# Kernel optimization log

Hardware: AMD Instinct MI355X
Metric: run time of the kernel (lower is better)

The kernel has to match this reference:

```python
import jax, jax.numpy as jnp
import numpy as np

B, S_ENC, S_DEC = 8, 128, 256
E, H = 256, 512
VE = VD = 32000


def _run_layer(x, h0, Wi, bi, Wh, bh):
    # Unidirectional Elman layer: h_t = tanh(i2h(x_t) + h2h(h_{t-1})).
    # i2h is time-independent, so precompute for all steps. x: [B,S,in]
    xi = jnp.einsum('bsi,hi->bsh', x, Wi) + bi
    def step(h, xt):
        h = jnp.tanh(xt + h @ Wh.T + bh)
        return h, h
    hT, ys = jax.lax.scan(step, h0, jnp.swapaxes(xi, 0, 1))
    return jnp.swapaxes(ys, 0, 1), hT  # [B,S,H], [B,H]


def _forward(enc_input, target, floats):
    (enc_emb, enc_Wi1, enc_bi1, enc_Wh1, enc_bh1, enc_Wi2, enc_bi2, enc_Wh2, enc_bh2,
     dec_emb, attn_We, attn_be, attn_Wh, attn_bh, attn_V, attn_bV,
     dec_Wi1, dec_bi1, dec_Wh1, dec_bh1, dec_Wi2, dec_bi2, dec_Wh2, dec_bh2,
     out_W, out_b) = floats
    b = enc_input.shape[0]
    # ---- encoder: 2-layer unidirectional Elman RNN over embedded tokens ----
    x = enc_emb[enc_input]                              # [B,S_enc,E]
    h0 = jnp.zeros((b, H), x.dtype)
    out1, h1 = _run_layer(x, h0, enc_Wi1, enc_bi1, enc_Wh1, enc_bh1)
    # RNNBlock passes layer1's final hidden as layer2's initial hidden
    enc_out, hidden = _run_layer(out1, h1, enc_Wi2, enc_bi2, enc_Wh2, enc_bh2)

    # ---- decoder with Bahdanau attention, teacher forcing always on ----
    # dec input at t=0 is target[:,0]; thereafter target[:,t-1]
    dec_tokens = jnp.concatenate([target[:, :1], target[:, :-1]], axis=1)
    dec_x = dec_emb[dec_tokens]                         # [B,S_dec,E]
    # W_enc_out(enc_output) is constant across decode steps -> precompute
    pre_enc = jnp.einsum('bsh,gh->bsg', enc_out, attn_We) + attn_be  # [B,S_enc,H]

    def dec_step(hidden, emb_t):
        align = jnp.tanh(pre_enc + (hidden @ attn_Wh.T + attn_bh)[:, None, :])
        dots = jnp.einsum('bsh,h->bs', align, attn_V[0]) + attn_bV[0]  # [B,S_enc]
        attn = jax.nn.softmax(dots, axis=-1)
        ctx = jnp.einsum('bs,bsh->bh', attn, enc_out)   # [B,H]
        x_t = jnp.concatenate([emb_t, ctx], axis=-1)    # [B,E+H]
        # decoder RNNBlock with seq_len=1: both layers start from `hidden`
        # chain per RNNBlock semantics (layer2 initial hidden = layer1 final)
        h1 = jnp.tanh(x_t @ dec_Wi1.T + dec_bi1 + hidden @ dec_Wh1.T + dec_bh1)
        h2 = jnp.tanh(h1 @ dec_Wi2.T + dec_bi2 + h1 @ dec_Wh2.T + dec_bh2)
        pred = h2 @ out_W.T + out_b                     # [B,VD]
        return h2, pred

    _, preds = jax.lax.scan(dec_step, hidden, jnp.swapaxes(dec_x, 0, 1))
    return jnp.swapaxes(preds, 0, 1)                    # [B,S_dec,VD]


def setup_inputs() -> dict:
    key = jax.random.key(0)
    it = iter(jax.random.split(key, 40))
    def nrm(shape, s=0.05):
        return (jax.random.normal(next(it), shape) * s).astype(jnp.float32)
    return dict(
        enc_input=jax.random.randint(next(it), (B, S_ENC), 0, VE),
        target=jax.random.randint(next(it), (B, S_DEC), 0, VD),
        enc_emb=nrm((VE, E)),
        enc_Wi1=nrm((H, E)), enc_bi1=nrm((H,)), enc_Wh1=nrm((H, H)), enc_bh1=nrm((H,)),
        enc_Wi2=nrm((H, H)), enc_bi2=nrm((H,)), enc_Wh2=nrm((H, H)), enc_bh2=nrm((H,)),
        dec_emb=nrm((VD, E)),
        attn_We=nrm((H, H)), attn_be=nrm((H,)), attn_Wh=nrm((H, H)), attn_bh=nrm((H,)),
        attn_V=nrm((1, H)), attn_bV=nrm((1,)),
        dec_Wi1=nrm((H, E + H)), dec_bi1=nrm((H,)), dec_Wh1=nrm((H, H)), dec_bh1=nrm((H,)),
        dec_Wi2=nrm((H, H)), dec_bi2=nrm((H,)), dec_Wh2=nrm((H, H)), dec_bh2=nrm((H,)),
        out_W=nrm((VD, H)), out_b=nrm((VD,)),
    )


def reference(enc_input, target, enc_emb, enc_Wi1, enc_bi1, enc_Wh1, enc_bh1,
              enc_Wi2, enc_bi2, enc_Wh2, enc_bh2, dec_emb,
              attn_We, attn_be, attn_Wh, attn_bh, attn_V, attn_bV,
              dec_Wi1, dec_bi1, dec_Wh1, dec_bh1, dec_Wi2, dec_bi2, dec_Wh2, dec_bh2,
              out_W, out_b):
    floats = (enc_emb, enc_Wi1, enc_bi1, enc_Wh1, enc_bh1, enc_Wi2, enc_bi2, enc_Wh2, enc_bh2,
              dec_emb, attn_We, attn_be, attn_Wh, attn_bh, attn_V, attn_bV,
              dec_Wi1, dec_bi1, dec_Wh1, dec_bh1, dec_Wi2, dec_bi2, dec_Wh2, dec_bh2,
              out_W, out_b)
    return _forward(enc_input, target, floats)
```

## Files before the change

kernel.cpp:

```cpp
#include <hip/hip_runtime.h>

#define TPB 256
#define NWG 32
#define B_  8
#define H_  512
#define E_  256
#define SE_ 128
#define SD_ 256
#define WS  530

typedef unsigned short u16;
typedef unsigned int   u32;
typedef __attribute__((ext_vector_type(4))) float f32x4;
typedef __attribute__((ext_vector_type(8))) short short8;
typedef __attribute__((ext_vector_type(2))) _Float16 half2v;

#define SENTU 0x7FC00001u

__device__ __forceinline__ u16 f2b(float f){
  u32 u = __float_as_uint(f);
  u = (u + 0x7fffu + ((u >> 16) & 1u)) >> 16;
  return (u16)u;
}
__device__ __forceinline__ u16 f2h(float f){
  _Float16 h = (_Float16)f;
  return __builtin_bit_cast(unsigned short, h);
}
__device__ __forceinline__ void b2f2(u32 p, float& a, float& b){
  a = __uint_as_float(p << 16);
  b = __uint_as_float(p & 0xffff0000u);
}
__device__ __forceinline__ float ftanh(float x){
  float e = __expf(2.f * x);
  return 1.f - 2.f / (e + 1.f);
}
__device__ __forceinline__ float red16(float v){
  v += __shfl_xor(v, 1); v += __shfl_xor(v, 2);
  v += __shfl_xor(v, 4); v += __shfl_xor(v, 8);
  return v;
}
__device__ __forceinline__ float sentf(){ return __uint_as_float(SENTU); }
__device__ __forceinline__ bool issent(float x){ return __float_as_uint(x) == SENTU; }
__device__ __forceinline__ float dot2h(half2v w, half2v x, float acc){
#if __has_builtin(__builtin_amdgcn_fdot2)
  return __builtin_amdgcn_fdot2(w, x, acc, false);
#else
  return acc + (float)w.x * (float)x.x + (float)w.y * (float)x.y;
#endif
}

__device__ __forceinline__ float gld(const float* p){
  return __hip_atomic_load(p, __ATOMIC_RELAXED, __HIP_MEMORY_SCOPE_AGENT);
}
__device__ __forceinline__ void gst(float* p, float v){
  __hip_atomic_store(p, v, __ATOMIC_RELAXED, __HIP_MEMORY_SCOPE_AGENT);
}

__device__ __forceinline__ int HPX(int slot,int b,int wg,int r){ return ((slot*8+b)*32+wg)*16+r; }
__device__ __forceinline__ int HPB(int slot,int b){ return (slot*8+b)*512; }
__device__ __forceinline__ int PPX(int slot,int b,int wg,int s){ return ((slot*8+b)*32+wg)*128+s; }
__device__ __forceinline__ int PPB(int slot,int b){ return (slot*8+b)*4096; }

__device__ __forceinline__ void pollgather_h(const float* base, half2v* dsth){
  const int tid = threadIdx.x;
  if (tid < 128){
    const float* p = base + tid*4;
    f32x4 v;
    for (;;){
      asm volatile("global_load_dwordx4 %0, %1, off sc0 sc1\n\ts_waitcnt vmcnt(0)"
                   : "=v"(v) : "v"(p) : "memory");
      bool ok = !issent(v.x) && !issent(v.y) && !issent(v.z) && !issent(v.w);
      if (__all(ok)) break;
      __builtin_amdgcn_s_sleep(1);
    }
    half2v h0, h1;
    h0.x = (_Float16)v.x; h0.y = (_Float16)v.y;
    h1.x = (_Float16)v.z; h1.y = (_Float16)v.w;
    dsth[tid*2]     = h0;
    dsth[tid*2 + 1] = h1;
  }
}

struct Inputs {
  const int   *enc_input, *target;
  const float *enc_emb;
  const float *enc_Wi1, *enc_bi1, *enc_Wh1, *enc_bh1;
  const float *enc_Wi2, *enc_bi2, *enc_Wh2, *enc_bh2;
  const float *dec_emb;
  const float *attn_We, *attn_be, *attn_Wh, *attn_bh, *attn_V, *attn_bV;
  const float *dec_Wi1, *dec_bi1, *dec_Wh1, *dec_bh1;
  const float *dec_Wi2, *dec_bi2, *dec_Wh2, *dec_bh2;
  const float *out_W, *out_b;
};
struct Wksp {
  u32*  bar;
  float *hbuf, *h1buf, *h2buf, *partials;
  float *xi1, *xi2, *out1, *encout, *xe;
  u16   *h2all, *wb;
};

constexpr int OFF_A   = 0;
constexpr int OFF_A2  = 17024;
constexpr int OFF_A3  = 34048;
constexpr int OFF_PM  = 51008;
constexpr int OFF_PES = 59200;
constexpr int OFF_STG = 67904;
constexpr int OFF_WRG = 76096;
constexpr int OFF_XVH = 125248;
constexpr int OFF_XV2H= 126272;
constexpr int OFF_ES  = 127296;
constexpr int OFF_QS  = 127808;
constexpr int OFF_VS  = 127872;
constexpr int OFF_B1  = 127936;
constexpr int OFF_B2  = 128000;
constexpr int OFF_BH  = 128064;
constexpr int OFF_BSC = 128128;
constexpr int OFF_SCR = 128192;
constexpr int LDS_BYTES = 128256;

__device__ __forceinline__ void cbar(u32* slots, int wg, u32 target){
  asm volatile("s_waitcnt vmcnt(0)" ::: "memory");
  __syncthreads();
  const int tid = threadIdx.x;
  if (tid < 64){
    if (tid == 0)
      __hip_atomic_store(&slots[wg], target, __ATOMIC_RELAXED, __HIP_MEMORY_SCOPE_AGENT);
    bool done = false;
    do {
      u32 v = __hip_atomic_load(&slots[tid & 31], __ATOMIC_RELAXED, __HIP_MEMORY_SCOPE_AGENT);
      done = (v >= target);
    } while (__ballot(done) != ~0ull);
  }
  __syncthreads();
  asm volatile("" ::: "memory");
}

__device__ void enc_scan(const Wksp& w,
                         const float* __restrict__ Wh, const float* __restrict__ bh,
                         const float* __restrict__ xi, float* __restrict__ outbuf,
                         int b, int wg, u16* WbE, half2v* xvh, float* bscan)
{
  const int tid = threadIdx.x;
  for (int i = tid; i < 16*512; i += TPB){
    int r = i >> 9, j = i & 511;
    WbE[r*WS + j] = f2h(Wh[((size_t)(wg*16 + r))*H_ + j]);
  }
  if (tid < 16) bscan[tid] = bh[wg*16 + tid];
  __syncthreads();
  for (int t = 0; t < SE_; t++){
    pollgather_h(&w.hbuf[HPB(t&3, b)], xvh);
    __syncthreads();
    int r = tid >> 4, sl = tid & 15;
    float acc = 0.f;
    #pragma unroll
    for (int k = 0; k < 16; k++){
      int jj = sl + 16*k;
      acc = dot2h(*(const half2v*)&WbE[r*WS + 2*jj], xvh[jj], acc);
    }
    acc = red16(acc);
    if (sl == 0){
      int row = wg*16 + r;
      float hv = ftanh(xi[((size_t)b*SE_ + t)*H_ + row] + acc + bscan[r]);
      gst(&w.hbuf[HPX((t+1)&3, b, wg, r)], hv);
      gst(&outbuf[((size_t)b*SE_ + t)*H_ + row], hv);
      gst(&w.hbuf[HPX((t+3)&3, b, wg, r)], sentf());
    }
    asm volatile("s_waitcnt vmcnt(0)" ::: "memory");
    __syncthreads();
  }
}

__global__ __launch_bounds__(TPB, 1) void seq2seq_persist(Inputs in, Wksp w)
{
  __shared__ __attribute__((aligned(16))) unsigned char S[LDS_BYTES];
  u16* Wh1s = (u16*)(S + OFF_A);
  u16* Ws2s = (u16*)(S + OFF_A2);
  u16* Wats = (u16*)(S + OFF_A3);
  u16* WaE  = (u16*)(S + OFF_A);
  u16* WbE  = (u16*)(S + OFF_A2);
  float* stgE = (float*)(S + OFF_A3);
  float* Pm   = (float*)(S + OFF_PM);
  float* pes  = (float*)(S + OFF_PES);
  float* STG  = (float*)(S + OFF_STG);
  float* WRG  = (float*)(S + OFF_WRG);
  half2v* xvh  = (half2v*)(S + OFF_XVH);
  half2v* xv2h = (half2v*)(S + OFF_XV2H);
  float* es   = (float*)(S + OFF_ES);
  float* qs   = (float*)(S + OFF_QS);
  float* Vs   = (float*)(S + OFF_VS);
  float* b1s  = (float*)(S + OFF_B1);
  float* b2s  = (float*)(S + OFF_B2);
  float* bhs  = (float*)(S + OFF_BH);
  float* bscan= (float*)(S + OFF_BSC);
  float* scr  = (float*)(S + OFF_SCR);

  const int bid = blockIdx.x;
  const int c = bid & 7, wg = bid >> 3;
  const int b = c;
  const int tid = threadIdx.x;
  u32* slots = w.bar + c*32;
  u32 bt = 0;

  if (tid < 16){
    gst(&w.hbuf[HPX(0, b, wg, tid)], 0.f);
    #pragma unroll
    for (int s2 = 1; s2 < 4; s2++) gst(&w.hbuf[HPX(s2, b, wg, tid)], sentf());
    #pragma unroll
    for (int s2 = 0; s2 < 4; s2++) gst(&w.h1buf[HPX(s2, b, wg, tid)], sentf());
    #pragma unroll
    for (int s2 = 0; s2 < 3; s2++) gst(&w.h2buf[HPX(s2, b, wg, tid)], sentf());
  }
  if (tid < 128){
    #pragma unroll
    for (int s2 = 0; s2 < 3; s2++) gst(&w.partials[PPX(s2, b, wg, tid)], sentf());
  }

  for (int i = tid; i < 16*256; i += TPB){
    int r = i >> 8, j = i & 255;
    WaE[r*264 + j] = f2b(in.enc_Wi1[((size_t)(wg*16 + r))*E_ + j]);
  }
  if (tid < 16) bscan[tid] = in.enc_bi1[wg*16 + tid];
  __syncthreads();
  for (int k0 = 0; k0 < 8; k0++){
    for (int it = 0; it < 16; it++){
      int tok = in.enc_input[b*SE_ + k0*16 + it];
      stgE[it*256 + tid] = in.enc_emb[(size_t)tok*E_ + tid];
    }
    __syncthreads();
    int r = tid & 15, tt = tid >> 4;
    float acc = 0.f;
    #pragma unroll 16
    for (int j = 0; j < 256; j += 2){
      u32 p = *(const u32*)&WaE[r*264 + j];
      float w0, w1; b2f2(p, w0, w1);
      float2 x = *(const float2*)&stgE[tt*256 + j];
      acc += w0*x.x + w1*x.y;
    }
    w.xi1[((size_t)b*SE_ + k0*16 + tt)*H_ + wg*16 + r] = acc + bscan[r];
    __syncthreads();
  }
  cbar(slots, wg, ++bt);

  enc_scan(w, in.enc_Wh1, in.enc_bh1, w.xi1, w.out1, b, wg, WbE, xvh, bscan);
  cbar(slots, wg, ++bt);

  for (int i = tid; i < 16*512; i += TPB){
    int r = i >> 9, j = i & 511;
    WaE[r*522 + j] = f2b(in.enc_Wi2[((size_t)(wg*16 + r))*H_ + j]);
  }
  if (tid < 16){
    bscan[tid] = in.enc_bi2[wg*16 + tid];
    #pragma unroll
    for (int s2 = 1; s2 < 4; s2++) gst(&w.hbuf[HPX(s2, b, wg, tid)], sentf());
  }
  __syncthreads();
  {
    u16* stg2 = (u16*)stgE;
    for (int k0 = 0; k0 < 8; k0++){
      for (int it = 0; it < 16; it++){
        size_t base = ((size_t)b*SE_ + k0*16 + it)*H_;
        stg2[it*512 + tid]       = f2b(gld(&w.out1[base + tid]));
        stg2[it*512 + tid + 256] = f2b(gld(&w.out1[base + tid + 256]));
      }
      __syncthreads();
      int r = tid & 15, tt = tid >> 4;
      float acc = 0.f;
      #pragma unroll 16
      for (int j = 0; j < 512; j += 2){
        u32 p  = *(const u32*)&WaE[r*522 + j];
        u32 s2 = *(const u32*)&stg2[tt*512 + j];
        float w0, w1, s0, s1; b2f2(p, w0, w1); b2f2(s2, s0, s1);
        acc += w0*s0 + w1*s1;
      }
      w.xi2[((size_t)b*SE_ + k0*16 + tt)*H_ + wg*16 + r] = acc + bscan[r];
      __syncthreads();
    }
  }
  cbar(slots, wg, ++bt);

  enc_scan(w, in.enc_Wh2, in.enc_bh2, w.xi2, w.encout, b, wg, WbE, xvh, bscan);
  cbar(slots, wg, ++bt);

  for (int i = tid; i < 16*768; i += TPB)
    WRG[i] = in.dec_Wi1[(size_t)(wg*16 + i/768)*768 + (i - (i/768)*768)];
  for (int tb = 0; tb < 32; tb++){
    __syncthreads();
    for (int i = tid; i < 8*256; i += TPB){
      int tt = tb*8 + (i >> 8);
      int tok = in.target[b*SD_ + (tt == 0 ? 0 : tt - 1)];
      STG[i] = in.dec_emb[(size_t)tok*E_ + (i & 255)];
    }
    __syncthreads();
    int r = tid >> 4, sl = tid & 15;
    for (int t2 = 0; t2 < 8; t2++){
      float acc = 0.f;
      #pragma unroll
      for (int k = 0; k < 8; k++){
        int j = 2*sl + 32*k;
        float2 wv = *(const float2*)&WRG[r*768 + j];
        float2 xx = *(const float2*)&STG[t2*256 + j];
        acc += wv.x*xx.x + wv.y*xx.y;
      }
      acc = red16(acc);
      if (sl == 0) w.xe[((size_t)b*SD_ + tb*8 + t2)*H_ + wg*16 + r] = acc;
    }
  }
  for (int sb = 0; sb < 32; sb++){
    __syncthreads();
    for (int i = tid; i < 4*512; i += TPB)
      STG[i] = gld(&w.encout[((size_t)b*SE_ + sb*4 + (i >> 9))*H_ + (i & 511)]);
    __syncthreads();
    int r = tid >> 4, sl = tid & 15;
    const float* wer = in.attn_We + (size_t)(wg*16 + r)*H_;
    float a0=0.f, a1=0.f, a2=0.f, a3=0.f;
    float p0=0.f, p1=0.f, p2=0.f, p3=0.f;
    #pragma unroll
    for (int k = 0; k < 16; k++){
      int j = 2*sl + 32*k;
      float2 wv = *(const float2*)&wer[j];
      float2 x0 = *(const float2*)&STG[j];
      float2 x1 = *(const float2*)&STG[512 + j];
      float2 x2 = *(const float2*)&STG[1024 + j];
      float2 x3 = *(const float2*)&STG[1536 + j];
      a0 += wv.x*x0.x + wv.y*x0.y;  a1 += wv.x*x1.x + wv.y*x1.y;
      a2 += wv.x*x2.x + wv.y*x2.y;  a3 += wv.x*x3.x + wv.y*x3.y;
      float2 cv = *(const float2*)&WRG[r*768 + 256 + j];
      p0 += cv.x*x0.x + cv.y*x0.y;  p1 += cv.x*x1.x + cv.y*x1.y;
      p2 += cv.x*x2.x + cv.y*x2.y;  p3 += cv.x*x3.x + cv.y*x3.y;
    }
    a0 = red16(a0); a1 = red16(a1); a2 = red16(a2); a3 = red16(a3);
    p0 = red16(p0); p1 = red16(p1); p2 = red16(p2); p3 = red16(p3);
    if (sl == 0){
      float bed = in.attn_be[wg*16 + r];
      pes[(sb*4 + 0)*17 + r] = a0 + bed;
      pes[(sb*4 + 1)*17 + r] = a1 + bed;
      pes[(sb*4 + 2)*17 + r] = a2 + bed;
      pes[(sb*4 + 3)*17 + r] = a3 + bed;
      Pm[r*128 + sb*4 + 0] = p0;  Pm[r*128 + sb*4 + 1] = p1;
      Pm[r*128 + sb*4 + 2] = p2;  Pm[r*128 + sb*4 + 3] = p3;
    }
  }
  __syncthreads();
  for (int i = tid; i < 16*512; i += TPB){
    int r = i >> 9, j = i & 511;
    size_t o = ((size_t)(wg*16 + r))*H_ + j;
    Wh1s[r*WS + j] = f2h(in.dec_Wh1[o]);
    Ws2s[r*WS + j] = f2h(in.dec_Wi2[o] + in.dec_Wh2[o]);
    Wats[r*WS + j] = f2h(in.attn_Wh[o]);
  }
  if (tid < 16){
    int row = wg*16 + tid;
    b1s[tid] = in.dec_bi1[row] + in.dec_bh1[row];
    b2s[tid] = in.dec_bi2[row] + in.dec_bh2[row];
    bhs[tid] = in.attn_bh[row];
    Vs[tid]  = in.attn_V[row];
    float hv = gld(&w.hbuf[HPX(0, b, wg, tid)]);
    gst(&w.h2buf[HPX(3, b, wg, tid)], hv);
  }
  if (tid == 0) scr[8] = in.attn_bV[0];
  cbar(slots, wg, ++bt);
  const float bVv = scr[8];

  {
    pollgather_h(&w.h2buf[HPB(3, b)], xv2h);
    __syncthreads();
    int r = tid >> 4, sl = tid & 15;
    float acc = 0.f;
    #pragma unroll
    for (int k = 0; k < 16; k++){
      int jj = sl + 16*k;
      acc = dot2h(*(const half2v*)&Wats[r*WS + 2*jj], xv2h[jj], acc);
    }
    acc = red16(acc);
    if (sl == 0) qs[r] = acc + bhs[r];
    __syncthreads();
    if (tid < 128){
      float part = 0.f;
      #pragma unroll
      for (int di = 0; di < 16; di++)
        part += Vs[di] * ftanh(pes[tid*17 + di] + qs[di]);
      gst(&w.partials[PPX(3, b, wg, tid)], part);
    }
  }
  cbar(slots, wg, ++bt);

  const int r = tid >> 4, sl = tid & 15;
  for (int t = 0; t < SD_; t++){
    const int sA = (t+3)&3;
    const int sB = t&3;
    const int sP = (t+1)&3;
    pollgather_h(&w.h2buf[HPB(sA, b)], xv2h);
    __syncthreads();
    {
      float aq = 0.f;
      #pragma unroll
      for (int k = 0; k < 16; k++){
        int jj = sl + 16*k;
        aq = dot2h(*(const half2v*)&Wats[r*WS + 2*jj], xv2h[jj], aq);
      }
      aq = red16(aq);
      if (sl == 0) qs[r] = aq + bhs[r];
    }
    __syncthreads();
    if (tid < 128){
      float part = 0.f;
      #pragma unroll
      for (int di = 0; di < 16; di++)
        part += Vs[di] * ftanh(pes[tid*17 + di] + qs[di]);
      gst(&w.partials[PPX(sA, b, wg, tid)], part);
    }
    float ah = 0.f;
    #pragma unroll
    for (int k = 0; k < 16; k++){
      int jj = sl + 16*k;
      ah = dot2h(*(const half2v*)&Wh1s[r*WS + 2*jj], xv2h[jj], ah);
    }
    if (tid < 128){
      const float* pb = &w.partials[PPB(sA, b)];
      float sum;
      for (;;){
        bool ok = true; sum = bVv;
        #pragma unroll
        for (int k = 0; k < 32; k++){
          float x = gld(pb + k*128 + tid);
          ok = ok && !issent(x);
          sum += x;
        }
        if (__all(ok)) break;
        __builtin_amdgcn_s_sleep(1);
      }
      float e = __expf(sum);
      es[tid] = e;
      float d = e;
      d += __shfl_xor(d, 1);  d += __shfl_xor(d, 2);  d += __shfl_xor(d, 4);
      d += __shfl_xor(d, 8);  d += __shfl_xor(d, 16); d += __shfl_xor(d, 32);
      if ((tid & 63) == 0) scr[tid >> 6] = d;
    }
    __syncthreads();
    {
      float rden = 1.f / (scr[0] + scr[1]);
      float accP = 0.f;
      #pragma unroll
      for (int k = 0; k < 8; k++){
        int s = sl + 16*k;
        accP += Pm[r*128 + s] * es[s];
      }
      float tot = red16(ah + accP*rden);
      if (sl == 0){
        int row = wg*16 + r;
        float h1v = ftanh(tot + w.xe[((size_t)b*SD_ + t)*H_ + row] + b1s[r]);
        gst(&w.h1buf[HPX(sB, b, wg, r)], h1v);
        gst(&w.h2buf[HPX(sP, b, wg, r)], sentf());
      }
      if (tid < 128)
        gst(&w.partials[PPX(sP, b, wg, tid)], sentf());
    }
    pollgather_h(&w.h1buf[HPB(sB, b)], xvh);
    __syncthreads();
    {
      float acc = 0.f;
      #pragma unroll
      for (int k = 0; k < 16; k++){
        int jj = sl + 16*k;
        acc = dot2h(*(const half2v*)&Ws2s[r*WS + 2*jj], xvh[jj], acc);
      }
      acc = red16(acc);
      if (sl == 0){
        float h2v = ftanh(acc + b2s[r]);
        int row = wg*16 + r;
        gst(&w.h2buf[HPX(sB, b, wg, r)], h2v);
        w.h2all[((size_t)(b*SD_ + t))*H_ + row] = f2b(h2v);
        gst(&w.h1buf[HPX((t+2)&3, b, wg, r)], sentf());
      }
    }
    asm volatile("s_waitcnt vmcnt(0)" ::: "memory");
    __syncthreads();
  }
}

__global__ void cvt_bf16(const float* __restrict__ src, u16* __restrict__ dst, int n4){
  int idx = blockIdx.x*blockDim.x + threadIdx.x;
  int stride = gridDim.x*blockDim.x;
  for (int i = idx; i < n4; i += stride){
    float4 v = ((const float4*)src)[i];
    ushort4 o;
    o.x = f2b(v.x); o.y = f2b(v.y); o.z = f2b(v.z); o.w = f2b(v.w);
    ((ushort4*)dst)[i] = o;
  }
}

__global__ __launch_bounds__(256, 1) void out_gemm(const u16* __restrict__ A,
    const u16* __restrict__ Bw, const float* __restrict__ bias, float* __restrict__ out)
{
  __shared__ u16 Al[128*32];
  __shared__ u16 Bl[128*32];
  int tid = threadIdx.x;
  int bidm = blockIdx.x & 15, bidn = blockIdx.x >> 4;
  int m0 = bidm*128, n0 = bidn*128;
  int wv = tid >> 6, l = tid & 63;
  int wm = wv >> 1, wn = wv & 1;
  f32x4 acc[4][4] = {};
  for (int k0 = 0; k0 < 512; k0 += 32){
    __syncthreads();
    #pragma unroll
    for (int rd = 0; rd < 2; rd++){
      int ci = rd*256 + wv*64 + l;
      int row = ci >> 2, qq = ci & 3;
      const u16* ga = A  + (size_t)(m0 + row)*512 + k0 + qq*8;
      const u16* gb = Bw + (size_t)(n0 + row)*512 + k0 + qq*8;
      __builtin_amdgcn_global_load_lds((const __attribute__((address_space(1))) unsigned int*)ga,
          (__attribute__((address_space(3))) unsigned int*)(Al + (rd*256 + wv*64)*8), 16, 0, 0);
      __builtin_amdgcn_global_load_lds((const __attribute__((address_space(1))) unsigned int*)gb,
          (__attribute__((address_space(3))) unsigned int*)(Bl + (rd*256 + wv*64)*8), 16, 0, 0);
    }
    __syncthreads();
    short8 af[4], bf[4];
    int lr = l & 15, lk = l >> 4;
    #pragma unroll
    for (int mi = 0; mi < 4; mi++)
      af[mi] = *(const short8*)(Al + (size_t)(wm*64 + mi*16 + lr)*32 + lk*8);
    #pragma unroll
    for (int ni = 0; ni < 4; ni++)
      bf[ni] = *(const short8*)(Bl + (size_t)(wn*64 + ni*16 + lr)*32 + lk*8);
    #pragma unroll
    for (int mi = 0; mi < 4; mi++)
      #pragma unroll
      for (int ni = 0; ni < 4; ni++)
        acc[mi][ni] = __builtin_amdgcn_mfma_f32_16x16x32_bf16(af[mi], bf[ni], acc[mi][ni], 0, 0, 0);
  }
  #pragma unroll
  for (int ni = 0; ni < 4; ni++){
    int col = n0 + wn*64 + ni*16 + (l & 15);
    float bb = bias[col];
    #pragma unroll
    for (int mi = 0; mi < 4; mi++){
      int row = m0 + wm*64 + mi*16 + (l >> 4)*4;
      #pragma unroll
      for (int r = 0; r < 4; r++)
        out[(size_t)(row + r)*32000 + col] = acc[mi][ni][r] + bb;
    }
  }
}

extern "C" void kernel_launch(void* const* d_in, const int* in_sizes, int n_in,
                              void* d_out, int out_size, void* d_ws, size_t ws_size,
                              hipStream_t stream)
{
  (void)in_sizes; (void)n_in; (void)out_size; (void)ws_size;
  Inputs in;
  in.enc_input = (const int*)d_in[0];
  in.target    = (const int*)d_in[1];
  in.enc_emb   = (const float*)d_in[2];
  in.enc_Wi1   = (const float*)d_in[3];  in.enc_bi1 = (const float*)d_in[4];
  in.enc_Wh1   = (const float*)d_in[5];  in.enc_bh1 = (const float*)d_in[6];
  in.enc_Wi2   = (const float*)d_in[7];  in.enc_bi2 = (const float*)d_in[8];
  in.enc_Wh2   = (const float*)d_in[9];  in.enc_bh2 = (const float*)d_in[10];
  in.dec_emb   = (const float*)d_in[11];
  in.attn_We   = (const float*)d_in[12]; in.attn_be = (const float*)d_in[13];
  in.attn_Wh   = (const float*)d_in[14]; in.attn_bh = (const float*)d_in[15];
  in.attn_V    = (const float*)d_in[16]; in.attn_bV = (const float*)d_in[17];
  in.dec_Wi1   = (const float*)d_in[18]; in.dec_bi1 = (const float*)d_in[19];
  in.dec_Wh1   = (const float*)d_in[20]; in.dec_bh1 = (const float*)d_in[21];
  in.dec_Wi2   = (const float*)d_in[22]; in.dec_bi2 = (const float*)d_in[23];
  in.dec_Wh2   = (const float*)d_in[24]; in.dec_bh2 = (const float*)d_in[25];
  in.out_W     = (const float*)d_in[26]; in.out_b   = (const float*)d_in[27];

  char* ws = (char*)d_ws;
  char* od = (char*)d_out;
  Wksp w;
  w.bar      = (u32*)ws;
  w.hbuf     = (float*)(ws + 1024);
  w.h1buf    = (float*)(ws + 66560);
  w.h2buf    = (float*)(ws + 132096);
  w.partials = (float*)(ws + 197632);
  w.h2all    = (u16*)  (ws + 721920);
  w.wb       = (u16*)  (ws + 2819072);
  w.xi1    = (float*)(od);
  w.xi2    = (float*)(od + (1 << 21));
  w.out1   = (float*)(od + 2*(1 << 21));
  w.encout = (float*)(od + 3*(1 << 21));
  w.xe     = (float*)(od + 4*(1 << 21));

  hipMemsetAsync(d_ws, 0, 1024, stream);
  cvt_bf16<<<dim3(4096), dim3(256), 0, stream>>>(in.out_W, w.wb, 32000*512/4);
  seq2seq_persist<<<dim3(256), dim3(TPB), 0, stream>>>(in, w);
  out_gemm<<<dim3(4000), dim3(256), 0, stream>>>(w.h2all, w.wb, in.out_b, (float*)d_out);
}
```

Baseline: 2.492 ms.

## Poll with all waves racing on an LDS done-flag and prefetch decoder input

Each cross-workgroup poll (hidden-state gather and attention partial sums) is now run by all four waves, staggered by s_sleep. Whichever wave first sees the data complete writes it to LDS and sets a shared LDS flag, so the other waves stop early. The aim is to cut the latency between a remote store landing and this workgroup noticing it, which matters on the serial recurrence critical path. The decoder's xe input is also loaded before the poll to hide its global latency. The cost is extra redundant polling traffic, plus reliance on volatile LDS flags and lgkmcnt ordering for correctness.

Result: slower. 2.969 ms (+19.1%).

```diff
diff --git a/kernel.cpp b/kernel.cpp
--- a/kernel.cpp
+++ b/kernel.cpp
@@ -48,6 +48,8 @@
   return acc + (float)w.x * (float)x.x + (float)w.y * (float)x.y;
 #endif
 }
+__device__ __forceinline__ float ldsflag(float* f){ return *(volatile float*)f; }
+__device__ __forceinline__ void stsflag(float* f, float v){ *(volatile float*)f = v; }
 
 __device__ __forceinline__ float gld(const float* p){
   return __hip_atomic_load(p, __ATOMIC_RELAXED, __HIP_MEMORY_SCOPE_AGENT);
@@ -61,24 +63,34 @@
 __device__ __forceinline__ int PPX(int slot,int b,int wg,int s){ return ((slot*8+b)*32+wg)*128+s; }
 __device__ __forceinline__ int PPB(int slot,int b){ return (slot*8+b)*4096; }
 
-__device__ __forceinline__ void pollgather_h(const float* base, half2v* dsth){
+__device__ __forceinline__ void pollgather_dual(const float* base, half2v* dsth, float* flg){
   const int tid = threadIdx.x;
-  if (tid < 128){
-    const float* p = base + tid*4;
-    f32x4 v;
-    for (;;){
-      asm volatile("global_load_dwordx4 %0, %1, off sc0 sc1\n\ts_waitcnt vmcnt(0)"
-                   : "=v"(v) : "v"(p) : "memory");
-      bool ok = !issent(v.x) && !issent(v.y) && !issent(v.z) && !issent(v.w);
-      if (__all(ok)) break;
-      __builtin_amdgcn_s_sleep(1);
-    }
-    half2v h0, h1;
-    h0.x = (_Float16)v.x; h0.y = (_Float16)v.y;
-    h1.x = (_Float16)v.z; h1.y = (_Float16)v.w;
-    dsth[tid*2]     = h0;
-    dsth[tid*2 + 1] = h1;
-  }
+  const int wv = tid >> 6, l = tid & 63;
+  if (wv == 1)      __builtin_amdgcn_s_sleep(6);
+  else if (wv == 2) __builtin_amdgcn_s_sleep(12);
+  else if (wv == 3) __builtin_amdgcn_s_sleep(18);
+  const float* p = base + l*8;
+  f32x4 v0, v1;
+  for (;;){
+    if (ldsflag(flg) != 0.f) return;
+    asm volatile("global_load_dwordx4 %0, %2, off sc0 sc1\n\t"
+                 "global_load_dwordx4 %1, %2, off offset:16 sc0 sc1\n\t"
+                 "s_waitcnt vmcnt(0)"
+                 : "=v"(v0), "=v"(v1) : "v"(p) : "memory");
+    bool ok = !issent(v0.x) & !issent(v0.y) & !issent(v0.z) & !issent(v0.w)
+            & !issent(v1.x) & !issent(v1.y) & !issent(v1.z) & !issent(v1.w);
+    if (__all(ok)) break;
+    __builtin_amdgcn_s_sleep(1);
+  }
+  half2v h0, h1, h2, h3;
+  h0.x = (_Float16)v0.x; h0.y = (_Float16)v0.y;
+  h1.x = (_Float16)v0.z; h1.y = (_Float16)v0.w;
+  h2.x = (_Float16)v1.x; h2.y = (_Float16)v1.y;
+  h3.x = (_Float16)v1.z; h3.y = (_Float16)v1.w;
+  dsth[l*4]     = h0; dsth[l*4 + 1] = h1;
+  dsth[l*4 + 2] = h2; dsth[l*4 + 3] = h3;
+  asm volatile("s_waitcnt lgkmcnt(0)" ::: "memory");
+  if (l == 0) stsflag(flg, 1.f);
 }
 
 struct Inputs {
@@ -138,7 +150,7 @@
 __device__ void enc_scan(const Wksp& w,
                          const float* __restrict__ Wh, const float* __restrict__ bh,
                          const float* __restrict__ xi, float* __restrict__ outbuf,
-                         int b, int wg, u16* WbE, half2v* xvh, float* bscan)
+                         int b, int wg, u16* WbE, half2v* xvh, float* bscan, float* flg)
 {
   const int tid = threadIdx.x;
   for (int i = tid; i < 16*512; i += TPB){
@@ -148,8 +160,9 @@
   if (tid < 16) bscan[tid] = bh[wg*16 + tid];
   __syncthreads();
   for (int t = 0; t < SE_; t++){
-    pollgather_h(&w.hbuf[HPB(t&3, b)], xvh);
-    __syncthreads();
+    pollgather_dual(&w.hbuf[HPB(t&3, b)], xvh, flg);
+    __syncthreads();
+    if (tid == 0) stsflag(flg, 0.f);
     int r = tid >> 4, sl = tid & 15;
     float acc = 0.f;
     #pragma unroll
@@ -193,6 +206,8 @@
   float* bhs  = (float*)(S + OFF_BH);
   float* bscan= (float*)(S + OFF_BSC);
   float* scr  = (float*)(S + OFF_SCR);
+  float* fH   = scr + 12;
+  float* fP   = scr + 13;
 
   const int bid = blockIdx.x;
   const int c = bid & 7, wg = bid >> 3;
@@ -201,6 +216,7 @@
   u32* slots = w.bar + c*32;
   u32 bt = 0;
 
+  if (tid == 0){ stsflag(fH, 0.f); stsflag(fP, 0.f); }
   if (tid < 16){
     gst(&w.hbuf[HPX(0, b, wg, tid)], 0.f);
     #pragma unroll
@@ -241,7 +257,7 @@
   }
   cbar(slots, wg, ++bt);
 
-  enc_scan(w, in.enc_Wh1, in.enc_bh1, w.xi1, w.out1, b, wg, WbE, xvh, bscan);
+  enc_scan(w, in.enc_Wh1, in.enc_bh1, w.xi1, w.out1, b, wg, WbE, xvh, bscan, fH);
   cbar(slots, wg, ++bt);
 
   for (int i = tid; i < 16*512; i += TPB){
@@ -278,7 +294,7 @@
   }
   cbar(slots, wg, ++bt);
 
-  enc_scan(w, in.enc_Wh2, in.enc_bh2, w.xi2, w.encout, b, wg, WbE, xvh, bscan);
+  enc_scan(w, in.enc_Wh2, in.enc_bh2, w.xi2, w.encout, b, wg, WbE, xvh, bscan, fH);
   cbar(slots, wg, ++bt);
 
   for (int i = tid; i < 16*768; i += TPB)
@@ -362,8 +378,9 @@
   const float bVv = scr[8];
 
   {
-    pollgather_h(&w.h2buf[HPB(3, b)], xv2h);
-    __syncthreads();
+    pollgather_dual(&w.h2buf[HPB(3, b)], xv2h, fH);
+    __syncthreads();
+    if (tid == 0) stsflag(fH, 0.f);
     int r = tid >> 4, sl = tid & 15;
     float acc = 0.f;
     #pragma unroll
@@ -389,8 +406,10 @@
     const int sA = (t+3)&3;
     const int sB = t&3;
     const int sP = (t+1)&3;
-    pollgather_h(&w.h2buf[HPB(sA, b)], xv2h);
-    __syncthreads();
+    float xepre = w.xe[((size_t)b*SD_ + t)*H_ + wg*16 + r];
+    pollgather_dual(&w.h2buf[HPB(sA, b)], xv2h, fH);
+    __syncthreads();
+    if (tid == 0) stsflag(fH, 0.f);
     {
       float aq = 0.f;
       #pragma unroll
@@ -415,30 +434,43 @@
       int jj = sl + 16*k;
       ah = dot2h(*(const half2v*)&Wh1s[r*WS + 2*jj], xv2h[jj], ah);
     }
-    if (tid < 128){
+    {
+      const int wv2 = tid >> 6, l2 = tid & 63;
+      if (wv2 == 1)      __builtin_amdgcn_s_sleep(6);
+      else if (wv2 == 2) __builtin_amdgcn_s_sleep(12);
+      else if (wv2 == 3) __builtin_amdgcn_s_sleep(18);
       const float* pb = &w.partials[PPB(sA, b)];
-      float sum;
       for (;;){
-        bool ok = true; sum = bVv;
+        if (ldsflag(fP) != 0.f) break;
+        bool ok = true; float sumA = bVv, sumB = bVv;
         #pragma unroll
         for (int k = 0; k < 32; k++){
-          float x = gld(pb + k*128 + tid);
-          ok = ok && !issent(x);
-          sum += x;
+          float xA = gld(pb + k*128 + l2);
+          float xB = gld(pb + k*128 + 64 + l2);
+          ok = ok & !issent(xA) & !issent(xB);
+          sumA += xA; sumB += xB;
         }
-        if (__all(ok)) break;
+        if (__all(ok)){
+          es[l2]      = __expf(sumA);
+          es[l2 + 64] = __expf(sumB);
+          asm volatile("s_waitcnt lgkmcnt(0)" ::: "memory");
+          if (l2 == 0) stsflag(fP, 1.f);
+          break;
+        }
         __builtin_amdgcn_s_sleep(1);
       }
-      float e = __expf(sum);
-      es[tid] = e;
-      float d = e;
+    }
+    __syncthreads();
+    if (tid == 0) stsflag(fP, 0.f);
+    if (tid < 64){
+      float d = es[tid] + es[tid + 64];
       d += __shfl_xor(d, 1);  d += __shfl_xor(d, 2);  d += __shfl_xor(d, 4);
       d += __shfl_xor(d, 8);  d += __shfl_xor(d, 16); d += __shfl_xor(d, 32);
-      if ((tid & 63) == 0) scr[tid >> 6] = d;
+      if (tid == 0) scr[0] = d;
     }
     __syncthreads();
     {
-      float rden = 1.f / (scr[0] + scr[1]);
+      float rden = 1.f / scr[0];
       float accP = 0.f;
       #pragma unroll
       for (int k = 0; k < 8; k++){
@@ -448,15 +480,16 @@
       float tot = red16(ah + accP*rden);
       if (sl == 0){
         int row = wg*16 + r;
-        float h1v = ftanh(tot + w.xe[((size_t)b*SD_ + t)*H_ + row] + b1s[r]);
+        float h1v = ftanh(tot + xepre + b1s[r]);
         gst(&w.h1buf[HPX(sB, b, wg, r)], h1v);
         gst(&w.h2buf[HPX(sP, b, wg, r)], sentf());
       }
       if (tid < 128)
         gst(&w.partials[PPX(sP, b, wg, tid)], sentf());
     }
-    pollgather_h(&w.h1buf[HPB(sB, b)], xvh);
-    __syncthreads();
+    pollgather_dual(&w.h1buf[HPB(sB, b)], xvh, fH);
+    __syncthreads();
+    if (tid == 0) stsflag(fH, 0.f);
     {
       float acc = 0.f;
       #pragma unroll
```
